# Performance work log

Hardware: AMD Instinct MI355X
Metric: run time of the kernel (lower is better)

Reference implementation:

```python
import jax, jax.numpy as jnp
import numpy as np

K = 3
STRIDE = 1
PADDING = 1
INVALID = -1.0


def _unfold(x, k, stride, padding, fill):
    # x: [B, C, H, W] -> patches [B, C, k, k, P] matching torch F.unfold ordering
    x = jnp.pad(x, ((0, 0), (0, 0), (padding, padding), (padding, padding)),
                constant_values=fill)
    # feature dim ordered channel-major (C, kh, kw), same as torch unfold
    p = jax.lax.conv_general_dilated_patches(x, (k, k), (stride, stride), 'VALID')
    b, _, ho, wo = p.shape
    c = x.shape[1]
    return p.reshape(b, c, k, k, ho * wo), ho, wo


def setup_inputs() -> dict:
    key = jax.random.key(0)
    k1, k2, k3, k4 = jax.random.split(key, 4)
    B, C, H, W = 8, 64, 128, 128
    OC = 64
    inp = jax.random.normal(k1, (B, C, H, W), dtype=jnp.float32)
    mask = jax.random.randint(k2, (B, H, W), 0, 4).astype(jnp.float32)
    conv = jax.random.normal(k3, (OC, C, K, K), dtype=jnp.float32) * 0.05
    bias = jax.random.normal(k4, (OC,), dtype=jnp.float32) * 0.05
    return {"inp": inp, "mask": mask, "conv": conv, "bias": bias}


def reference(inp, mask, conv, bias):
    k, stride, padding = K, STRIDE, PADDING
    b, c, h_in, w_in = inp.shape
    oc = conv.shape[0]
    center = (k - 1) // 2

    inp_patched, ho, wo = _unfold(inp, k, stride, padding, INVALID)       # [B,C,k,k,P]
    mask_patched, _, _ = _unfold(mask[:, None], k, stride, padding, INVALID)  # [B,1,k,k,P]
    mask_patched = mask_patched[:, 0]                                      # [B,k,k,P]

    center_val = mask_patched[:, center:center + 1, center:center + 1, :]  # [B,1,1,P]
    mask_eq = (mask_patched == center_val).astype(inp.dtype)               # [B,k,k,P]

    masked_input = inp_patched * mask_eq[:, None]                          # [B,C,k,k,P]
    m_norm = (k * k) / jnp.clip(mask_eq.reshape(b, k * k, -1).sum(axis=1), 1e-8)  # [B,P]

    masked_input = masked_input.reshape(b, c, k * k, -1)                   # [B,C,kk,P]
    w = conv.reshape(oc, c, k * k)                                         # [O,C,kk]
    out = jnp.einsum('bcxp,ocx->bop', masked_input, w)                     # [B,O,P]
    out = out * m_norm[:, None, :]
    out = out.reshape(b, oc, ho, wo)
    out = out + bias[None, :, None, None]

    mask_out = mask_patched[:, center, center, :].reshape(b, 1, ho, wo)
    return out, mask_out
```

## Files before the change

### kernel.cpp

```cpp
#include <hip/hip_runtime.h>
#include <stdint.h>

#define HW   128
#define CIN  64
#define OCN  64
#define NB   8

typedef __attribute__((ext_vector_type(8)))  short short8;
typedef __attribute__((ext_vector_type(16))) float floatx16;

union F8 { short8 s; uint32_t d[4]; uint4 q; };

static __device__ __forceinline__ ushort f2bf(float f) {
    uint32_t u = __float_as_uint(f);
    return (ushort)((u + 0x7FFFu + ((u >> 16) & 1u)) >> 16);
}

__global__ __launch_bounds__(256)
void wprep_kernel(const float* __restrict__ conv, ushort* __restrict__ wb2) {
    int idx = blockIdx.x * 256 + threadIdx.x;
    int j  = idx & 7;
    int l  = (idx >> 3) & 63;
    int h  = (idx >> 9) & 1;
    int ks = (idx >> 10) & 3;
    int t  = idx >> 12;
    int oc = (l & 31) + h * 32;
    int c  = ks * 16 + (l >> 5) * 8 + j;
    wb2[idx] = f2bf(conv[(oc * 64 + c) * 9 + t]);
}

#define LDS_BYTES 65536

__global__ __launch_bounds__(256, 2)
void iconv_main(const float* __restrict__ inp, const ushort* __restrict__ wb2,
                const float* __restrict__ mask, const float* __restrict__ bias,
                float* __restrict__ out)
{
    extern __shared__ char smem[];
    ushort* Ls = (ushort*)smem;

    const int tid  = threadIdx.x;
    const int bb   = blockIdx.x >> 6;
    const int y0   = (blockIdx.x & 63) << 1;
    const int lane = tid & 63, l31 = lane & 31, lh = lane >> 5;
    const int w    = tid >> 6;
    const int yloc = w >> 1, xh = w & 1;
    const int y    = y0 + yloc, xw = xh * 64;
    const int x0   = xw + l31, x1 = x0 + 32;

    {
        const int cg = tid & 7, xg = tid >> 3;
        #pragma unroll
        for (int rr = 0; rr < 4; ++rr) {
            int gy = y0 - 1 + rr;
            gy = gy < 0 ? 0 : (gy > HW - 1 ? HW - 1 : gy);
            const float* src = inp + ((size_t)(bb * CIN + cg * 8) * HW + gy) * HW + xg * 4;
            float4 v[8];
            #pragma unroll
            for (int k = 0; k < 8; ++k)
                v[k] = *(const float4*)(src + (size_t)k * HW * HW);
            const float* fv = (const float*)v;
            ushort* lrow = Ls + rr * 8192;
            #pragma unroll
            for (int j = 0; j < 4; ++j) {
                int px = xg * 4 + j;
                uint32_t d0 = (uint32_t)f2bf(fv[0 * 4 + j]) | ((uint32_t)f2bf(fv[1 * 4 + j]) << 16);
                uint32_t d1 = (uint32_t)f2bf(fv[2 * 4 + j]) | ((uint32_t)f2bf(fv[3 * 4 + j]) << 16);
                uint32_t d2 = (uint32_t)f2bf(fv[4 * 4 + j]) | ((uint32_t)f2bf(fv[5 * 4 + j]) << 16);
                uint32_t d3 = (uint32_t)f2bf(fv[6 * 4 + j]) | ((uint32_t)f2bf(fv[7 * 4 + j]) << 16);
                int slot = cg ^ (px & 7);
                *(uint4*)(lrow + px * 64 + slot * 8) = make_uint4(d0, d1, d2, d3);
            }
        }
    }

    const float* mrow = mask + ((size_t)bb * HW + y) * HW;
    const float m00 = mrow[x0], m01 = mrow[x1];
    uint32_t bits0 = 0, bits1 = 0;
    #pragma unroll
    for (int t = 0; t < 9; ++t) {
        int dy = t / 3 - 1, dx = t % 3 - 1;
        int ny = y + dy;
        bool vy = (ny >= 0) && (ny < HW);
        int nyc = vy ? ny : y;
        const float* r = mask + ((size_t)bb * HW + nyc) * HW;
        int nx0 = x0 + dx, nx1 = x1 + dx;
        bool ok0 = vy && (nx0 >= 0) && (nx0 < HW);
        bool ok1 = vy && (nx1 >= 0) && (nx1 < HW);
        int c0 = nx0 < 0 ? 0 : (nx0 > HW - 1 ? HW - 1 : nx0);
        int c1 = nx1 < 0 ? 0 : (nx1 > HW - 1 ? HW - 1 : nx1);
        if (ok0 && r[c0] == m00) bits0 |= 1u << t;
        if (ok1 && r[c1] == m01) bits1 |= 1u << t;
    }
    const float norm0 = 9.0f / (float)__popc(bits0);
    const float norm1 = 9.0f / (float)__popc(bits1);

    float* mout = out + (size_t)NB * OCN * HW * HW + ((size_t)bb * HW + y) * HW;
    mout[x0] = m00;
    mout[x1] = m01;

    uint4 Ar[2][8];
    #pragma unroll
    for (int i = 0; i < 8; ++i) {
        int ks = i >> 1, h = i & 1;
        Ar[0][h * 4 + ks] = *(const uint4*)(wb2 + (size_t)i * 512 + lane * 8);
    }

    __syncthreads();

    floatx16 acc00 = {0,0,0,0,0,0,0,0,0,0,0,0,0,0,0,0};
    floatx16 acc01 = {0,0,0,0,0,0,0,0,0,0,0,0,0,0,0,0};
    floatx16 acc10 = {0,0,0,0,0,0,0,0,0,0,0,0,0,0,0,0};
    floatx16 acc11 = {0,0,0,0,0,0,0,0,0,0,0,0,0,0,0,0};

    #pragma unroll
    for (int t = 0; t < 9; ++t) {
        const int buf = t & 1;
        if (t < 8) {
            const ushort* wp = wb2 + (size_t)(t + 1) * 4096;
            #pragma unroll
            for (int i = 0; i < 8; ++i) {
                int ks = i >> 1, h = i & 1;
                Ar[buf ^ 1][h * 4 + ks] = *(const uint4*)(wp + (size_t)i * 512 + lane * 8);
            }
        }

        const int dy = t / 3 - 1, dx = t % 3 - 1;
        const int rrB = 1 + yloc + dy;
        int p0 = x0 + dx; p0 = p0 < 0 ? 0 : (p0 > HW - 1 ? HW - 1 : p0);
        int p1 = x1 + dx; p1 = p1 < 0 ? 0 : (p1 > HW - 1 ? HW - 1 : p1);
        const ushort* b0b = Ls + rrB * 8192 + p0 * 64;
        const ushort* b1b = Ls + rrB * 8192 + p1 * 64;
        const int sw0 = p0 & 7, sw1 = p1 & 7;
        const uint32_t s0 = ((bits0 >> t) & 1u) ? 0xFFFFFFFFu : 0u;
        const uint32_t s1 = ((bits1 >> t) & 1u) ? 0xFFFFFFFFu : 0u;

        #pragma unroll
        for (int ks = 0; ks < 4; ++ks) {
            F8 a0, a1, b0, b1;
            a0.q = Ar[buf][ks];
            a1.q = Ar[buf][4 + ks];
            b0.q = *(const uint4*)(b0b + (((2 * ks + lh) ^ sw0) * 8));
            b1.q = *(const uint4*)(b1b + (((2 * ks + lh) ^ sw1) * 8));
            b0.d[0] &= s0; b0.d[1] &= s0; b0.d[2] &= s0; b0.d[3] &= s0;
            b1.d[0] &= s1; b1.d[1] &= s1; b1.d[2] &= s1; b1.d[3] &= s1;
            acc00 = __builtin_amdgcn_mfma_f32_32x32x16_bf16(a0.s, b0.s, acc00, 0, 0, 0);
            acc01 = __builtin_amdgcn_mfma_f32_32x32x16_bf16(a0.s, b1.s, acc01, 0, 0, 0);
            acc10 = __builtin_amdgcn_mfma_f32_32x32x16_bf16(a1.s, b0.s, acc10, 0, 0, 0);
            acc11 = __builtin_amdgcn_mfma_f32_32x32x16_bf16(a1.s, b1.s, acc11, 0, 0, 0);
        }
    }

    float* outp = out + (size_t)bb * OCN * HW * HW + (size_t)y * HW;
    #pragma unroll
    for (int mt = 0; mt < 2; ++mt) {
        #pragma unroll
        for (int nt = 0; nt < 2; ++nt) {
            floatx16 a = (mt == 0) ? (nt == 0 ? acc00 : acc01)
                                   : (nt == 0 ? acc10 : acc11);
            float nm = (nt == 0) ? norm0 : norm1;
            int x = xw + nt * 32 + l31;
            #pragma unroll
            for (int r = 0; r < 16; ++r) {
                int oc = mt * 32 + (r & 3) + 8 * (r >> 2) + 4 * lh;
                outp[(size_t)oc * (HW * HW) + x] = a[r] * nm + bias[oc];
            }
        }
    }
}

extern "C" void kernel_launch(void* const* d_in, const int* in_sizes, int n_in,
                              void* d_out, int out_size, void* d_ws, size_t ws_size,
                              hipStream_t stream) {
    (void)in_sizes; (void)n_in; (void)out_size; (void)ws_size;
    const float* inp  = (const float*)d_in[0];
    const float* mask = (const float*)d_in[1];
    const float* conv = (const float*)d_in[2];
    const float* bias = (const float*)d_in[3];
    float* out = (float*)d_out;

    ushort* wb2 = (ushort*)d_ws;

    hipFuncSetAttribute((const void*)iconv_main,
                        hipFuncAttributeMaxDynamicSharedMemorySize, LDS_BYTES);

    wprep_kernel<<<144, 256, 0, stream>>>(conv, wb2);
    iconv_main<<<NB * (HW / 2), 256, LDS_BYTES, stream>>>(inp, wb2, mask, bias, out);
}
```

Measured before the change: 106.2 us.

## Split output channels across 8 waves per block and interleave batch in grid

Each block now has 512 threads. The extra four waves each compute one half of the output channels, so every wave holds 2 accumulators instead of 4 and loads half the weight fragments. This cuts register pressure and doubles the waves available to hide latency. Staging of the input rows into LDS is split across both halves. Block index ordering now interleaves the batch in the low bits, which changes the L2 access pattern. The cost is duplicated mask computation and B-fragment LDS reads across the two halves. The launch-bounds value of 4 blocks of 512 threads may also not fit with 64KB of LDS per block.

```diff
diff --git a/kernel.cpp b/kernel.cpp
--- a/kernel.cpp
+++ b/kernel.cpp
@@ -31,7 +31,7 @@
 
 #define LDS_BYTES 65536
 
-__global__ __launch_bounds__(256, 2)
+__global__ __launch_bounds__(512, 4)
 void iconv_main(const float* __restrict__ inp, const ushort* __restrict__ wb2,
                 const float* __restrict__ mask, const float* __restrict__ bias,
                 float* __restrict__ out)
@@ -40,18 +40,20 @@
     ushort* Ls = (ushort*)smem;
 
     const int tid  = threadIdx.x;
-    const int bb   = blockIdx.x >> 6;
-    const int y0   = (blockIdx.x & 63) << 1;
+    const int bb   = blockIdx.x & 7;
+    const int y0   = (blockIdx.x >> 3) << 1;
     const int lane = tid & 63, l31 = lane & 31, lh = lane >> 5;
     const int w    = tid >> 6;
-    const int yloc = w >> 1, xh = w & 1;
+    const int h    = w >> 2;
+    const int yloc = (w >> 1) & 1, xh = w & 1;
     const int y    = y0 + yloc, xw = xh * 64;
     const int x0   = xw + l31, x1 = x0 + 32;
 
     {
-        const int cg = tid & 7, xg = tid >> 3;
+        const int cg = tid & 7, xg = (tid >> 3) & 31, rh = tid >> 8;
         #pragma unroll
-        for (int rr = 0; rr < 4; ++rr) {
+        for (int r = 0; r < 2; ++r) {
+            int rr = rh * 2 + r;
             int gy = y0 - 1 + rr;
             gy = gy < 0 ? 0 : (gy > HW - 1 ? HW - 1 : gy);
             const float* src = inp + ((size_t)(bb * CIN + cg * 8) * HW + gy) * HW + xg * 4;
@@ -95,23 +97,21 @@
     const float norm0 = 9.0f / (float)__popc(bits0);
     const float norm1 = 9.0f / (float)__popc(bits1);
 
-    float* mout = out + (size_t)NB * OCN * HW * HW + ((size_t)bb * HW + y) * HW;
-    mout[x0] = m00;
-    mout[x1] = m01;
+    if (h == 0) {
+        float* mout = out + (size_t)NB * OCN * HW * HW + ((size_t)bb * HW + y) * HW;
+        mout[x0] = m00;
+        mout[x1] = m01;
+    }
 
-    uint4 Ar[2][8];
+    uint4 Ar[2][4];
     #pragma unroll
-    for (int i = 0; i < 8; ++i) {
-        int ks = i >> 1, h = i & 1;
-        Ar[0][h * 4 + ks] = *(const uint4*)(wb2 + (size_t)i * 512 + lane * 8);
-    }
+    for (int ks = 0; ks < 4; ++ks)
+        Ar[0][ks] = *(const uint4*)(wb2 + (size_t)((ks * 2 + h) * 512) + lane * 8);
 
     __syncthreads();
 
-    floatx16 acc00 = {0,0,0,0,0,0,0,0,0,0,0,0,0,0,0,0};
-    floatx16 acc01 = {0,0,0,0,0,0,0,0,0,0,0,0,0,0,0,0};
-    floatx16 acc10 = {0,0,0,0,0,0,0,0,0,0,0,0,0,0,0,0};
-    floatx16 acc11 = {0,0,0,0,0,0,0,0,0,0,0,0,0,0,0,0};
+    floatx16 acc0 = {0,0,0,0,0,0,0,0,0,0,0,0,0,0,0,0};
+    floatx16 acc1 = {0,0,0,0,0,0,0,0,0,0,0,0,0,0,0,0};
 
     #pragma unroll
     for (int t = 0; t < 9; ++t) {
@@ -119,10 +119,8 @@
         if (t < 8) {
             const ushort* wp = wb2 + (size_t)(t + 1) * 4096;
             #pragma unroll
-            for (int i = 0; i < 8; ++i) {
-                int ks = i >> 1, h = i & 1;
-                Ar[buf ^ 1][h * 4 + ks] = *(const uint4*)(wp + (size_t)i * 512 + lane * 8);
-            }
+            for (int ks = 0; ks < 4; ++ks)
+                Ar[buf ^ 1][ks] = *(const uint4*)(wp + (ks * 2 + h) * 512 + lane * 8);
         }
 
         const int dy = t / 3 - 1, dx = t % 3 - 1;
@@ -137,34 +135,27 @@
 
         #pragma unroll
         for (int ks = 0; ks < 4; ++ks) {
-            F8 a0, a1, b0, b1;
-            a0.q = Ar[buf][ks];
-            a1.q = Ar[buf][4 + ks];
+            F8 a, b0, b1;
+            a.q  = Ar[buf][ks];
             b0.q = *(const uint4*)(b0b + (((2 * ks + lh) ^ sw0) * 8));
             b1.q = *(const uint4*)(b1b + (((2 * ks + lh) ^ sw1) * 8));
             b0.d[0] &= s0; b0.d[1] &= s0; b0.d[2] &= s0; b0.d[3] &= s0;
             b1.d[0] &= s1; b1.d[1] &= s1; b1.d[2] &= s1; b1.d[3] &= s1;
-            acc00 = __builtin_amdgcn_mfma_f32_32x32x16_bf16(a0.s, b0.s, acc00, 0, 0, 0);
-            acc01 = __builtin_amdgcn_mfma_f32_32x32x16_bf16(a0.s, b1.s, acc01, 0, 0, 0);
-            acc10 = __builtin_amdgcn_mfma_f32_32x32x16_bf16(a1.s, b0.s, acc10, 0, 0, 0);
-            acc11 = __builtin_amdgcn_mfma_f32_32x32x16_bf16(a1.s, b1.s, acc11, 0, 0, 0);
+            acc0 = __builtin_amdgcn_mfma_f32_32x32x16_bf16(a.s, b0.s, acc0, 0, 0, 0);
+            acc1 = __builtin_amdgcn_mfma_f32_32x32x16_bf16(a.s, b1.s, acc1, 0, 0, 0);
         }
     }
 
     float* outp = out + (size_t)bb * OCN * HW * HW + (size_t)y * HW;
     #pragma unroll
-    for (int mt = 0; mt < 2; ++mt) {
+    for (int nt = 0; nt < 2; ++nt) {
+        floatx16 a = nt == 0 ? acc0 : acc1;
+        float nm   = nt == 0 ? norm0 : norm1;
+        int x = xw + nt * 32 + l31;
         #pragma unroll
-        for (int nt = 0; nt < 2; ++nt) {
-            floatx16 a = (mt == 0) ? (nt == 0 ? acc00 : acc01)
-                                   : (nt == 0 ? acc10 : acc11);
-            float nm = (nt == 0) ? norm0 : norm1;
-            int x = xw + nt * 32 + l31;
-            #pragma unroll
-            for (int r = 0; r < 16; ++r) {
-                int oc = mt * 32 + (r & 3) + 8 * (r >> 2) + 4 * lh;
-                outp[(size_t)oc * (HW * HW) + x] = a[r] * nm + bias[oc];
-            }
+        for (int r = 0; r < 16; ++r) {
+            int oc = h * 32 + (r & 3) + 8 * (r >> 2) + 4 * lh;
+            outp[(size_t)oc * (HW * HW) + x] = a[r] * nm + bias[oc];
         }
     }
 }
@@ -185,5 +176,5 @@
                         hipFuncAttributeMaxDynamicSharedMemorySize, LDS_BYTES);
 
     wprep_kernel<<<144, 256, 0, stream>>>(conv, wb2);
-    iconv_main<<<NB * (HW / 2), 256, LDS_BYTES, stream>>>(inp, wb2, mask, bias, out);
+    iconv_main<<<NB * (HW / 2), 512, LDS_BYTES, stream>>>(inp, wb2, mask, bias, out);
 }
```

After: 106.2 us. About the same (-0.0%).
